# Kernel tuning notes

Measured on AMD Instinct MI355X. Metric: run time of the kernel, lower is better.

## Reference

```python
import jax, jax.numpy as jnp
import numpy as np

N_NODES = 100000
N_EDGES = 3200000
F_IN = 512
HIDDEN = 16
N_CLASSES = 64
EPS = 1e-12  # F.normalize eps


def agnn_layer(x, src, dst, beta, n_nodes):
    """AGNNConv: cosine-similarity attention + segment softmax + scatter aggregate.
    x: [N, H]; src/dst: [E] (messages flow src -> dst, softmax over edges per dst).
    """
    norm = jnp.sqrt(jnp.sum(x * x, axis=-1, keepdims=True))
    xn = x / jnp.maximum(norm, EPS)                      # L2-normalized features
    cos = jnp.sum(xn[src] * xn[dst], axis=-1)            # [E] cosine similarity
    logits = beta * cos
    m = jax.ops.segment_max(logits, dst, num_segments=n_nodes)   # stable softmax per dst
    e = jnp.exp(logits - m[dst])
    denom = jax.ops.segment_sum(e, dst, num_segments=n_nodes)
    alpha = e / denom[dst]                               # [E]
    return jax.ops.segment_sum(alpha[:, None] * x[src], dst, num_segments=n_nodes)


def setup_inputs() -> dict:
    key = jax.random.key(0)
    ks = jax.random.split(key, 6)
    x = jax.random.normal(ks[0], (N_NODES, F_IN), dtype=jnp.float32)
    edge_index = jax.random.randint(ks[1], (2, N_EDGES), 0, N_NODES, dtype=jnp.int64)
    W1 = jax.random.normal(ks[2], (F_IN, HIDDEN), dtype=jnp.float32) * (1.0 / np.sqrt(F_IN))
    b1 = jnp.zeros((HIDDEN,), dtype=jnp.float32)
    W2 = jax.random.normal(ks[3], (HIDDEN, N_CLASSES), dtype=jnp.float32) * (1.0 / np.sqrt(HIDDEN))
    b2 = jnp.zeros((N_CLASSES,), dtype=jnp.float32)
    beta1 = jnp.ones((), dtype=jnp.float32)  # AGNNConv beta init = 1.0
    beta2 = jnp.ones((), dtype=jnp.float32)
    return {"x": x, "edge_index": edge_index, "W1": W1, "b1": b1,
            "W2": W2, "b2": b2, "beta1": beta1, "beta2": beta2}


def reference(x, edge_index, W1, b1, W2, b2, beta1, beta2):
    n = x.shape[0]
    # PyG AGNNConv adds self-loops before propagation
    loops = jnp.arange(n, dtype=edge_index.dtype)
    src = jnp.concatenate([edge_index[0], loops])
    dst = jnp.concatenate([edge_index[1], loops])
    # eval mode: dropout is identity
    h = jax.nn.relu(x @ W1 + b1)                 # [N, 16]
    h = agnn_layer(h, src, dst, beta1, n)
    h = agnn_layer(h, src, dst, beta2, n)
    out = h @ W2 + b2                            # [N, num_classes]
    return jax.nn.log_softmax(out, axis=1)
```

## Files before the change

### kernel.cpp

```cpp
#include <hip/hip_runtime.h>
#include <hip/hip_bf16.h>

#define F_IN 512
#define HID 16
#define NCLS 64
#define NBUCK_MAX 512
#define EPB 8192

__global__ __launch_bounds__(256) void gemm1_kernel(
    const float* __restrict__ x, const float* __restrict__ W1,
    const float* __restrict__ b1, float* __restrict__ h0,
    float* __restrict__ inv0, int N, int totalWaves)
{
    int wid  = (blockIdx.x * blockDim.x + threadIdx.x) >> 6;
    int lane = threadIdx.x & 63;
    float bias = b1[lane & 15];
    bool s3 = (lane & 8) != 0;
    bool s2 = (lane & 4) != 0;
    bool s1 = (lane & 2) != 0;
    bool s0 = (lane & 1) != 0;

    for (int row = wid; row < N; row += totalWaves) {
        const float4* xp = (const float4*)(x + (size_t)row * F_IN + 8 * lane);
        float4 ta = xp[0], tb = xp[1];
        float xv[8] = {ta.x, ta.y, ta.z, ta.w, tb.x, tb.y, tb.z, tb.w};

        float acc[16];
#pragma unroll
        for (int i = 0; i < 16; ++i) acc[i] = 0.f;

#pragma unroll
        for (int kk = 0; kk < 8; ++kk) {
            const float4* wp = (const float4*)(W1 + (size_t)(8 * lane + kk) * HID);
            float xs = xv[kk];
#pragma unroll
            for (int jj = 0; jj < 4; ++jj) {
                float4 t = wp[jj];
                acc[jj * 4 + 0] += xs * t.x;
                acc[jj * 4 + 1] += xs * t.y;
                acc[jj * 4 + 2] += xs * t.z;
                acc[jj * 4 + 3] += xs * t.w;
            }
        }

#pragma unroll
        for (int i = 0; i < 8; ++i) {
            float k = s3 ? acc[i + 8] : acc[i];
            float s = s3 ? acc[i] : acc[i + 8];
            acc[i] = k + __shfl_xor(s, 8);
        }
#pragma unroll
        for (int i = 0; i < 4; ++i) {
            float k = s2 ? acc[i + 4] : acc[i];
            float s = s2 ? acc[i] : acc[i + 4];
            acc[i] = k + __shfl_xor(s, 4);
        }
#pragma unroll
        for (int i = 0; i < 2; ++i) {
            float k = s1 ? acc[i + 2] : acc[i];
            float s = s1 ? acc[i] : acc[i + 2];
            acc[i] = k + __shfl_xor(s, 2);
        }
        {
            float k = s0 ? acc[1] : acc[0];
            float s = s0 ? acc[0] : acc[1];
            acc[0] = k + __shfl_xor(s, 1);
        }
        acc[0] += __shfl_xor(acc[0], 16);
        acc[0] += __shfl_xor(acc[0], 32);

        float val = fmaxf(acc[0] + bias, 0.f);
        if (lane < 16) h0[(size_t)row * HID + lane] = val;

        float q = val * val;
        q += __shfl_xor(q, 1);
        q += __shfl_xor(q, 2);
        q += __shfl_xor(q, 4);
        q += __shfl_xor(q, 8);
        if (lane == 0) inv0[row] = 1.f / fmaxf(sqrtf(q), 1e-12f);
    }
}

__global__ __launch_bounds__(256) void hist1_kernel(
    const int* __restrict__ dst, int E, int EV, int nbuck,
    int* __restrict__ bucketCount)
{
    __shared__ int h[NBUCK_MAX];
    int tid = threadIdx.x;
    for (int j = tid; j < nbuck; j += 256) h[j] = 0;
    __syncthreads();
    int base = blockIdx.x * EPB;
    for (int k = 0; k < EPB / 256; ++k) {
        int i = base + k * 256 + tid;
        if (i < EV) {
            int d = (i < E) ? dst[i] : (i - E);
            atomicAdd(&h[d >> 8], 1);
        }
    }
    __syncthreads();
    for (int j = tid; j < nbuck; j += 256)
        if (h[j]) atomicAdd(&bucketCount[j], h[j]);
}

__global__ __launch_bounds__(512) void bucket_scan_kernel(
    const int* __restrict__ bucketCount, int nbuck,
    int* __restrict__ bucketStart, int* __restrict__ gCursor)
{
    __shared__ int s[512];
    int t = threadIdx.x;
    int v = (t < nbuck) ? bucketCount[t] : 0;
    s[t] = v;
    __syncthreads();
    for (int off = 1; off < 512; off <<= 1) {
        int add = (t >= off) ? s[t - off] : 0;
        __syncthreads();
        s[t] += add;
        __syncthreads();
    }
    int incl = s[t];
    if (t < nbuck) {
        bucketStart[t] = incl - v;
        gCursor[t]     = incl - v;
        if (t == nbuck - 1) bucketStart[nbuck] = incl;
    }
}

__global__ __launch_bounds__(256) void partition_kernel(
    const int* __restrict__ src, const int* __restrict__ dst,
    int E, int EV, int nbuck, int* __restrict__ gCursor,
    unsigned* __restrict__ staged)
{
    __shared__ int h[NBUCK_MAX];
    __shared__ int gb[NBUCK_MAX];
    int tid = threadIdx.x;
    for (int j = tid; j < nbuck; j += 256) h[j] = 0;
    __syncthreads();

    unsigned pk[EPB / 256];
    int      bk[EPB / 256];
    int base = blockIdx.x * EPB;
#pragma unroll
    for (int k = 0; k < EPB / 256; ++k) {
        int i = base + k * 256 + tid;
        if (i < EV) {
            int s, d;
            if (i < E) { s = src[i]; d = dst[i]; }
            else       { s = i - E;  d = s; }
            bk[k] = d >> 8;
            pk[k] = (unsigned)s | ((unsigned)(d & 255) << 17);
            atomicAdd(&h[bk[k]], 1);
        } else {
            bk[k] = -1;
        }
    }
    __syncthreads();
    for (int j = tid; j < nbuck; j += 256) {
        int c = h[j];
        if (c) gb[j] = atomicAdd(&gCursor[j], c);
        h[j] = 0;
    }
    __syncthreads();
#pragma unroll
    for (int k = 0; k < EPB / 256; ++k) {
        if (bk[k] >= 0) {
            int ofs = atomicAdd(&h[bk[k]], 1);
            staged[gb[bk[k]] + ofs] = pk[k];
        }
    }
}

__global__ __launch_bounds__(256) void build_csr_kernel(
    const unsigned* __restrict__ staged, const int* __restrict__ bucketStart,
    int* __restrict__ counts, int* __restrict__ rowstart,
    int* __restrict__ esrc, int N)
{
    __shared__ int hist[256];
    __shared__ int s[256];
    __shared__ int cur[256];
    int b   = blockIdx.x;
    int tid = threadIdx.x;
    int start = bucketStart[b];
    int end   = bucketStart[b + 1];

    hist[tid] = 0;
    __syncthreads();
    for (int i = start + tid; i < end; i += 256)
        atomicAdd(&hist[(staged[i] >> 17) & 255], 1);
    __syncthreads();

    int v = hist[tid];
    s[tid] = v;
    __syncthreads();
    for (int off = 1; off < 256; off <<= 1) {
        int add = (tid >= off) ? s[tid - off] : 0;
        __syncthreads();
        s[tid] += add;
        __syncthreads();
    }
    int excl = s[tid] - v;
    int dstg = b * 256 + tid;
    if (dstg < N) {
        counts[dstg]   = v;
        rowstart[dstg] = start + excl;
    }
    cur[tid] = start + excl;
    __syncthreads();

    for (int i = start + tid; i < end; i += 256) {
        unsigned pk = staged[i];
        int dl  = (pk >> 17) & 255;
        int pos = atomicAdd(&cur[dl], 1);
        esrc[pos] = (int)(pk & 0x1FFFFu);
    }
}

__global__ __launch_bounds__(256) void agg_kernel(
    const float* __restrict__ h, const float* __restrict__ inv,
    const int* __restrict__ esrc, const int* __restrict__ rowstart,
    const int* __restrict__ counts, const float* __restrict__ beta_p,
    float* __restrict__ hout, float* __restrict__ invout, int N)
{
    int node = (blockIdx.x * blockDim.x + threadIdx.x) >> 6;
    if (node >= N) return;
    int lane = threadIdx.x & 63;
    int j = lane & 15;

    float beta  = *beta_p;
    float shift = fabsf(beta);
    float hd   = h[(size_t)node * HID + j];
    float invd = inv[node];
    int start = rowstart[node];
    int cnt   = counts[node];

    float denom = 0.f, acc = 0.f;
    for (int t = (lane >> 4); t < cnt; t += 4) {
        int s    = esrc[start + t];
        float hs = h[(size_t)s * HID + j];
        float p  = hs * hd;
        p += __shfl_xor(p, 1);
        p += __shfl_xor(p, 2);
        p += __shfl_xor(p, 4);
        p += __shfl_xor(p, 8);
        float w = __expf(beta * (p * invd * inv[s]) - shift);
        denom += w;
        acc   += w * hs;
    }
    denom += __shfl_xor(denom, 16);
    denom += __shfl_xor(denom, 32);
    acc   += __shfl_xor(acc, 16);
    acc   += __shfl_xor(acc, 32);

    float o = acc / denom;
    if (lane < 16) hout[(size_t)node * HID + j] = o;

    float q = o * o;
    q += __shfl_xor(q, 1);
    q += __shfl_xor(q, 2);
    q += __shfl_xor(q, 4);
    q += __shfl_xor(q, 8);
    if (lane == 0) invout[node] = 1.f / fmaxf(sqrtf(q), 1e-12f);
}

__global__ __launch_bounds__(256) void out_kernel(
    const float* __restrict__ h2, const float* __restrict__ W2,
    const float* __restrict__ b2, float* __restrict__ out, int N)
{
    int wave = (blockIdx.x * blockDim.x + threadIdx.x) >> 6;
    int lane = threadIdx.x & 63;
    if (wave >= N) return;

    float hv = (lane < HID) ? h2[(size_t)wave * HID + lane] : 0.f;
    float acc = b2[lane];
#pragma unroll
    for (int k = 0; k < HID; ++k) {
        float hk = __shfl(hv, k);
        acc += hk * W2[k * NCLS + lane];
    }
    float m = acc;
    for (int off = 32; off > 0; off >>= 1) m = fmaxf(m, __shfl_xor(m, off));
    float e = __expf(acc - m);
    float ssum = e;
    for (int off = 32; off > 0; off >>= 1) ssum += __shfl_xor(ssum, off);
    out[(size_t)wave * NCLS + lane] = (acc - m) - __logf(ssum);
}

extern "C" void kernel_launch(void* const* d_in, const int* in_sizes, int n_in,
                              void* d_out, int out_size, void* d_ws, size_t ws_size,
                              hipStream_t stream)
{
    const float* x     = (const float*)d_in[0];
    const int*   eidx  = (const int*)d_in[1];
    const float* W1    = (const float*)d_in[2];
    const float* b1    = (const float*)d_in[3];
    const float* W2    = (const float*)d_in[4];
    const float* b2    = (const float*)d_in[5];
    const float* beta1 = (const float*)d_in[6];
    const float* beta2 = (const float*)d_in[7];

    int N = in_sizes[0] / F_IN;
    int E = in_sizes[1] / 2;
    const int* src = eidx;
    const int* dst = eidx + E;
    float* out = (float*)d_out;

    int EV    = E + N;
    int nbuck = (N + 255) / 256;

    char* wptr = (char*)d_ws;
    auto alloc = [&](size_t bytes) -> char* {
        char* p = wptr;
        wptr += (bytes + 255) / 256 * 256;
        return p;
    };
    float*    h0       = (float*)alloc((size_t)N * HID * 4);
    float*    inv0     = (float*)alloc((size_t)N * 4);
    float*    h1       = (float*)alloc((size_t)N * HID * 4);
    float*    inv1     = (float*)alloc((size_t)N * 4);
    float*    h2       = (float*)alloc((size_t)N * HID * 4);
    float*    inv2     = (float*)alloc((size_t)N * 4);
    int*      counts   = (int*)alloc((size_t)N * 4);
    int*      rowstart = (int*)alloc((size_t)(N + 1) * 4);
    int*      esrc     = (int*)alloc((size_t)EV * 4);
    unsigned* staged   = (unsigned*)alloc((size_t)EV * 4);
    int*      bucketCount = (int*)alloc((size_t)(nbuck + 1) * 4);
    int*      bucketStart = (int*)alloc((size_t)(nbuck + 1) * 4);
    int*      gCursor     = (int*)alloc((size_t)nbuck * 4);

    int ebBlocks = (EV + EPB - 1) / EPB;

    hipMemsetAsync(bucketCount, 0, (size_t)nbuck * 4, stream);
    hist1_kernel<<<ebBlocks, 256, 0, stream>>>(dst, E, EV, nbuck, bucketCount);
    bucket_scan_kernel<<<1, 512, 0, stream>>>(bucketCount, nbuck, bucketStart, gCursor);
    partition_kernel<<<ebBlocks, 256, 0, stream>>>(src, dst, E, EV, nbuck, gCursor, staged);
    build_csr_kernel<<<nbuck, 256, 0, stream>>>(staged, bucketStart, counts, rowstart,
                                                esrc, N);

    int g1blocks = 2048;
    gemm1_kernel<<<g1blocks, 256, 0, stream>>>(x, W1, b1, h0, inv0, N, g1blocks * 4);

    int aggBlocks = (N + 3) / 4;
    agg_kernel<<<aggBlocks, 256, 0, stream>>>(h0, inv0, esrc, rowstart, counts, beta1,
                                              h1, inv1, N);
    agg_kernel<<<aggBlocks, 256, 0, stream>>>(h1, inv1, esrc, rowstart, counts, beta2,
                                              h2, inv2, N);

    out_kernel<<<(N * 64 + 255) / 256, 256, 0, stream>>>(h2, W2, b2, out, N);
}
```

Before: 666.3 us.

## Vectorize AGNN aggregation to 16 edges per wave, recompute partition keys

The aggregation kernel now has each lane load a float4 slice of the neighbor row, so 16 edges are processed per wave iteration instead of 4. This cuts the shuffle reductions per edge and widens the memory transactions. The partition kernel drops its per-thread register arrays and re-reads src and dst in a second pass instead. That lowers register pressure but doubles the global reads of dst.

```diff
diff --git a/kernel.cpp b/kernel.cpp
--- a/kernel.cpp
+++ b/kernel.cpp
@@ -136,35 +136,30 @@
     for (int j = tid; j < nbuck; j += 256) h[j] = 0;
     __syncthreads();
 
-    unsigned pk[EPB / 256];
-    int      bk[EPB / 256];
     int base = blockIdx.x * EPB;
-#pragma unroll
+    for (int k = 0; k < EPB / 256; ++k) {
+        int i = base + k * 256 + tid;
+        if (i < EV) {
+            int d = (i < E) ? dst[i] : (i - E);
+            atomicAdd(&h[d >> 8], 1);
+        }
+    }
+    __syncthreads();
+    for (int j = tid; j < nbuck; j += 256) {
+        int c = h[j];
+        if (c) gb[j] = atomicAdd(&gCursor[j], c);
+        h[j] = 0;
+    }
+    __syncthreads();
     for (int k = 0; k < EPB / 256; ++k) {
         int i = base + k * 256 + tid;
         if (i < EV) {
             int s, d;
             if (i < E) { s = src[i]; d = dst[i]; }
             else       { s = i - E;  d = s; }
-            bk[k] = d >> 8;
-            pk[k] = (unsigned)s | ((unsigned)(d & 255) << 17);
-            atomicAdd(&h[bk[k]], 1);
-        } else {
-            bk[k] = -1;
-        }
-    }
-    __syncthreads();
-    for (int j = tid; j < nbuck; j += 256) {
-        int c = h[j];
-        if (c) gb[j] = atomicAdd(&gCursor[j], c);
-        h[j] = 0;
-    }
-    __syncthreads();
-#pragma unroll
-    for (int k = 0; k < EPB / 256; ++k) {
-        if (bk[k] >= 0) {
-            int ofs = atomicAdd(&h[bk[k]], 1);
-            staged[gb[bk[k]] + ofs] = pk[k];
+            int bkt = d >> 8;
+            int ofs = atomicAdd(&h[bkt], 1);
+            staged[gb[bkt] + ofs] = (unsigned)s | ((unsigned)(d & 255) << 17);
         }
     }
 }
@@ -223,42 +218,48 @@
     int node = (blockIdx.x * blockDim.x + threadIdx.x) >> 6;
     if (node >= N) return;
     int lane = threadIdx.x & 63;
-    int j = lane & 15;
+    int q = lane & 3;
+    int e = lane >> 2;
 
     float beta  = *beta_p;
     float shift = fabsf(beta);
-    float hd   = h[(size_t)node * HID + j];
-    float invd = inv[node];
+    float4 hd4  = ((const float4*)(h + (size_t)node * HID))[q];
+    float  invd = inv[node];
     int start = rowstart[node];
     int cnt   = counts[node];
 
-    float denom = 0.f, acc = 0.f;
-    for (int t = (lane >> 4); t < cnt; t += 4) {
-        int s    = esrc[start + t];
-        float hs = h[(size_t)s * HID + j];
-        float p  = hs * hd;
+    float denom = 0.f;
+    float4 acc = make_float4(0.f, 0.f, 0.f, 0.f);
+    for (int t = e; t < cnt; t += 16) {
+        int s = esrc[start + t];
+        float4 hs4 = ((const float4*)(h + (size_t)s * HID))[q];
+        float invs = inv[s];
+        float p = hs4.x * hd4.x + hs4.y * hd4.y + hs4.z * hd4.z + hs4.w * hd4.w;
         p += __shfl_xor(p, 1);
         p += __shfl_xor(p, 2);
-        p += __shfl_xor(p, 4);
-        p += __shfl_xor(p, 8);
-        float w = __expf(beta * (p * invd * inv[s]) - shift);
+        float w = __expf(beta * (p * invd * invs) - shift);
         denom += w;
-        acc   += w * hs;
-    }
-    denom += __shfl_xor(denom, 16);
-    denom += __shfl_xor(denom, 32);
-    acc   += __shfl_xor(acc, 16);
-    acc   += __shfl_xor(acc, 32);
-
-    float o = acc / denom;
-    if (lane < 16) hout[(size_t)node * HID + j] = o;
-
-    float q = o * o;
-    q += __shfl_xor(q, 1);
-    q += __shfl_xor(q, 2);
-    q += __shfl_xor(q, 4);
-    q += __shfl_xor(q, 8);
-    if (lane == 0) invout[node] = 1.f / fmaxf(sqrtf(q), 1e-12f);
+        acc.x += w * hs4.x;
+        acc.y += w * hs4.y;
+        acc.z += w * hs4.z;
+        acc.w += w * hs4.w;
+    }
+#pragma unroll
+    for (int off = 4; off <= 32; off <<= 1) {
+        denom += __shfl_xor(denom, off);
+        acc.x += __shfl_xor(acc.x, off);
+        acc.y += __shfl_xor(acc.y, off);
+        acc.z += __shfl_xor(acc.z, off);
+        acc.w += __shfl_xor(acc.w, off);
+    }
+    float rd = 1.f / denom;
+    float4 o = make_float4(acc.x * rd, acc.y * rd, acc.z * rd, acc.w * rd);
+    if (lane < 4) ((float4*)(hout + (size_t)node * HID))[q] = o;
+
+    float ss = o.x * o.x + o.y * o.y + o.z * o.z + o.w * o.w;
+    ss += __shfl_xor(ss, 1);
+    ss += __shfl_xor(ss, 2);
+    if (lane == 0) invout[node] = 1.f / fmaxf(sqrtf(ss), 1e-12f);
 }
 
 __global__ __launch_bounds__(256) void out_kernel(
```

Measured after the change: 584.9 us. 12.2% less time.
